# Kernel optimization log

Measured on AMD Instinct MI355X. Metric: run time of the kernel, lower is better.

## Reference

```python
import jax, jax.numpy as jnp
import numpy as np

TAU = 2.0
V_TH = 1.0
V_RESET = 0.0


def setup_inputs() -> dict:
    key = jax.random.key(0)
    k1, k2 = jax.random.split(key)
    T, N, C, H, W = 16, 8, 64, 64, 64
    x_seq = jax.random.normal(k1, (T, N, C, H, W), dtype=jnp.float32)
    conv_weight = jax.random.normal(k2, (C, C, 3, 3), dtype=jnp.float32) * 0.05
    return {"x_seq": x_seq, "conv_weight": conv_weight}


def _conv2d(x, w):
    # x: (B, C, H, W), w: (Cout, Cin, 3, 3), padding=1, no bias
    return jax.lax.conv_general_dilated(
        x, w, window_strides=(1, 1), padding=((1, 1), (1, 1)),
        dimension_numbers=("NCHW", "OIHW", "NCHW"))


def _lif_scan(z_seq):
    # z_seq: (T, N, C, H, W); LIF: decay_input=True, hard reset to V_RESET.
    def step(v, x):
        # charge: v = v + (x - (v - v_reset)) / tau
        v = v + (x - (v - V_RESET)) / TAU
        s = (v >= V_TH).astype(v.dtype)
        # hard reset: v = (1 - s) * v + s * v_reset
        v = (1.0 - s) * v + s * V_RESET
        return v, s

    v0 = jnp.full(z_seq.shape[1:], V_RESET, dtype=z_seq.dtype)
    _, spikes = jax.lax.scan(step, v0, z_seq)
    return spikes


def reference(x_seq, conv_weight):
    T, N = x_seq.shape[:2]
    z = _conv2d(x_seq.reshape(T * N, *x_seq.shape[2:]), conv_weight)
    z = z.reshape(T, N, *z.shape[1:])
    return _lif_scan(z)
```

## Files before the change

kernel.cpp:

```cpp
#include <hip/hip_runtime.h>


namespace {
constexpr int T = 16, N = 8, C = 64, H = 64, W = 64;
constexpr int HW   = H * W;
constexpr int CHW  = C * HW;
constexpr int NCHW = N * CHW;
constexpr int NWT  = C * C * 9;
}

__global__ void wtr_kernel(const float* __restrict__ w, float* __restrict__ wt2) {
    int i = blockIdx.x * 256 + threadIdx.x;
    if (i >= NWT) return;
    int tap  = i % 9;
    int rem  = i / 9;
    int ci   = rem % 64;
    int cout = rem / 64;
    wt2[(tap * 64 + ci) * 64 + cout] = w[i];
}

__global__ __launch_bounds__(256, 6) void conv_kernel(
    const float* __restrict__ x,
    const float* __restrict__ wt2,
    float*       __restrict__ zo)
{
#pragma clang fp contract(off)
    __shared__ float xs[16 * 400];

    const int tid  = threadIdx.x;
    const int wave = __builtin_amdgcn_readfirstlane(tid >> 6);
    const int lane = tid & 63;
    const int px = lane & 7;
    const int py = lane >> 3;
    const int c0 = wave << 4;

    const int bid  = blockIdx.x;
    const int t    = bid >> 9;
    const int r    = bid & 511;
    const int n    = r >> 6;
    const int tile = r & 63;
    const int th0 = (tile >> 3) << 3;
    const int tw0 = (tile & 7) << 3;

    const float* xt = x + (size_t)(t * N + n) * CHW;

#pragma unroll
    for (int it = 0; it < 25; ++it) {
        int j  = tid + it * 256;
        int ci = j / 100;
        int rr = j - ci * 100;
        int dy = rr / 10;
        int dx = rr - dy * 10;
        int hh = th0 - 1 + dy;
        int ww = tw0 - 1 + dx;
        float val = 0.0f;
        if ((unsigned)hh < (unsigned)H && (unsigned)ww < (unsigned)W)
            val = xt[ci * HW + hh * W + ww];
        xs[(ci >> 2) * 400 + rr * 4 + (ci & 3)] = val;
    }
    __syncthreads();

    float acc[16];
#pragma unroll
    for (int i = 0; i < 16; ++i) acc[i] = 0.0f;

    for (int tap = 0; tap < 9; ++tap) {
        const int ky = tap / 3, kx = tap - 3 * ky;
        const int pos = (py + ky) * 10 + (px + kx);
        const float4* xp = (const float4*)xs + pos;
        const float* wtap = wt2 + tap * 4096 + c0;
#pragma unroll 2
        for (int cib = 0; cib < 16; ++cib) {
            const float4 xv = xp[cib * 100];
            const float* wp = wtap + cib * 256;
#pragma unroll
            for (int cc = 0; cc < 16; ++cc)
                acc[cc] = fmaf(wp[cc], xv.x, acc[cc]);
#pragma unroll
            for (int cc = 0; cc < 16; ++cc)
                acc[cc] = fmaf(wp[64 + cc], xv.y, acc[cc]);
#pragma unroll
            for (int cc = 0; cc < 16; ++cc)
                acc[cc] = fmaf(wp[128 + cc], xv.z, acc[cc]);
#pragma unroll
            for (int cc = 0; cc < 16; ++cc)
                acc[cc] = fmaf(wp[192 + cc], xv.w, acc[cc]);
        }
    }

    float* zt = zo + (size_t)(t * N + n) * CHW;
    const int pbase = (th0 + py) * W + (tw0 + px);
#pragma unroll
    for (int cc = 0; cc < 16; ++cc)
        zt[(c0 + cc) * HW + pbase] = acc[cc];
}

__global__ void lif_kernel(float* __restrict__ zo) {
#pragma clang fp contract(off)
    const int gid = blockIdx.x * 256 + threadIdx.x;
    float4 v;
    v.x = 0.0f; v.y = 0.0f; v.z = 0.0f; v.w = 0.0f;
#pragma unroll
    for (int t = 0; t < T; ++t) {
        float4* p = (float4*)(zo + (size_t)t * NCHW) + gid;
        float4 z = *p;
        float4 s;
#define LIF_STEP(comp) { float d = z.comp - v.comp; float hh = d * 0.5f;      \
        v.comp = v.comp + hh;                                                  \
        if (v.comp >= 1.0f) { s.comp = 1.0f; v.comp = 0.0f; }                  \
        else                { s.comp = 0.0f; } }
        LIF_STEP(x) LIF_STEP(y) LIF_STEP(z) LIF_STEP(w)
#undef LIF_STEP
        *p = s;
    }
}

extern "C" void kernel_launch(void* const* d_in, const int* in_sizes, int n_in,
                              void* d_out, int out_size, void* d_ws, size_t ws_size,
                              hipStream_t stream) {
    const float* x = (const float*)d_in[0];
    const float* w = (const float*)d_in[1];
    if (n_in >= 2 && in_sizes[0] < in_sizes[1]) {
        const float* tmp = x; x = w; w = tmp;
    }
    float* out = (float*)d_out;
    float* wt2 = (float*)d_ws;

    wtr_kernel<<<(NWT + 255) / 256, 256, 0, stream>>>(w, wt2);
    conv_kernel<<<T * N * 64, 256, 0, stream>>>(x, wt2, out);
    lif_kernel<<<NCHW / 1024, 256, 0, stream>>>(out);
}
```

Before: 665.1 us.

## Widen conv tile to 8x16 pixels per block and process two float4 per LIF thread

The conv kernel now computes two pixels per thread (8x16 tile per block, half as many blocks), so each weight value loaded is reused across two accumulator sets. This halves weight loads per FMA and reduces halo overhead in shared memory. The cost is higher register pressure (32 accumulators), with launch bounds lowered to 3 blocks per SM. The LIF kernel also gives each thread two float4 streams to raise memory-level parallelism with half the blocks.

```diff
diff --git a/kernel.cpp b/kernel.cpp
--- a/kernel.cpp
+++ b/kernel.cpp
@@ -7,6 +7,7 @@
 constexpr int CHW  = C * HW;
 constexpr int NCHW = N * CHW;
 constexpr int NWT  = C * C * 9;
+constexpr int NPOS = 10 * 18;
 }
 
 __global__ void wtr_kernel(const float* __restrict__ w, float* __restrict__ wt2) {
@@ -19,13 +20,13 @@
     wt2[(tap * 64 + ci) * 64 + cout] = w[i];
 }
 
-__global__ __launch_bounds__(256, 6) void conv_kernel(
+__global__ __launch_bounds__(256, 3) void conv_kernel(
     const float* __restrict__ x,
     const float* __restrict__ wt2,
     float*       __restrict__ zo)
 {
 #pragma clang fp contract(off)
-    __shared__ float xs[16 * 400];
+    __shared__ float xs[16 * NPOS * 4];
 
     const int tid  = threadIdx.x;
     const int wave = __builtin_amdgcn_readfirstlane(tid >> 6);
@@ -35,83 +36,108 @@
     const int c0 = wave << 4;
 
     const int bid  = blockIdx.x;
-    const int t    = bid >> 9;
-    const int r    = bid & 511;
-    const int n    = r >> 6;
-    const int tile = r & 63;
-    const int th0 = (tile >> 3) << 3;
-    const int tw0 = (tile & 7) << 3;
+    const int t    = bid >> 8;
+    const int r    = bid & 255;
+    const int n    = r >> 5;
+    const int tile = r & 31;
+    const int th0 = (tile >> 2) << 3;
+    const int tw0 = (tile & 3) << 4;
 
     const float* xt = x + (size_t)(t * N + n) * CHW;
 
 #pragma unroll
-    for (int it = 0; it < 25; ++it) {
+    for (int it = 0; it < 45; ++it) {
         int j  = tid + it * 256;
-        int ci = j / 100;
-        int rr = j - ci * 100;
-        int dy = rr / 10;
-        int dx = rr - dy * 10;
+        int ci = j / NPOS;
+        int rr = j - ci * NPOS;
+        int dy = rr / 18;
+        int dx = rr - dy * 18;
         int hh = th0 - 1 + dy;
         int ww = tw0 - 1 + dx;
         float val = 0.0f;
         if ((unsigned)hh < (unsigned)H && (unsigned)ww < (unsigned)W)
             val = xt[ci * HW + hh * W + ww];
-        xs[(ci >> 2) * 400 + rr * 4 + (ci & 3)] = val;
+        xs[(ci >> 2) * (NPOS * 4) + rr * 4 + (ci & 3)] = val;
     }
     __syncthreads();
 
-    float acc[16];
+    float acc0[16], acc1[16];
 #pragma unroll
-    for (int i = 0; i < 16; ++i) acc[i] = 0.0f;
+    for (int i = 0; i < 16; ++i) { acc0[i] = 0.0f; acc1[i] = 0.0f; }
 
     for (int tap = 0; tap < 9; ++tap) {
         const int ky = tap / 3, kx = tap - 3 * ky;
-        const int pos = (py + ky) * 10 + (px + kx);
+        const int pos = (py + ky) * 18 + (px + kx);
         const float4* xp = (const float4*)xs + pos;
         const float* wtap = wt2 + tap * 4096 + c0;
 #pragma unroll 2
         for (int cib = 0; cib < 16; ++cib) {
-            const float4 xv = xp[cib * 100];
+            const float4 xv0 = xp[cib * NPOS];
+            const float4 xv1 = xp[cib * NPOS + 8];
             const float* wp = wtap + cib * 256;
 #pragma unroll
-            for (int cc = 0; cc < 16; ++cc)
-                acc[cc] = fmaf(wp[cc], xv.x, acc[cc]);
+            for (int cc = 0; cc < 16; ++cc) {
+                float w0 = wp[cc];
+                acc0[cc] = fmaf(w0, xv0.x, acc0[cc]);
+                acc1[cc] = fmaf(w0, xv1.x, acc1[cc]);
+            }
 #pragma unroll
-            for (int cc = 0; cc < 16; ++cc)
-                acc[cc] = fmaf(wp[64 + cc], xv.y, acc[cc]);
+            for (int cc = 0; cc < 16; ++cc) {
+                float w1 = wp[64 + cc];
+                acc0[cc] = fmaf(w1, xv0.y, acc0[cc]);
+                acc1[cc] = fmaf(w1, xv1.y, acc1[cc]);
+            }
 #pragma unroll
-            for (int cc = 0; cc < 16; ++cc)
-                acc[cc] = fmaf(wp[128 + cc], xv.z, acc[cc]);
+            for (int cc = 0; cc < 16; ++cc) {
+                float w2 = wp[128 + cc];
+                acc0[cc] = fmaf(w2, xv0.z, acc0[cc]);
+                acc1[cc] = fmaf(w2, xv1.z, acc1[cc]);
+            }
 #pragma unroll
-            for (int cc = 0; cc < 16; ++cc)
-                acc[cc] = fmaf(wp[192 + cc], xv.w, acc[cc]);
+            for (int cc = 0; cc < 16; ++cc) {
+                float w3 = wp[192 + cc];
+                acc0[cc] = fmaf(w3, xv0.w, acc0[cc]);
+                acc1[cc] = fmaf(w3, xv1.w, acc1[cc]);
+            }
         }
     }
 
     float* zt = zo + (size_t)(t * N + n) * CHW;
     const int pbase = (th0 + py) * W + (tw0 + px);
 #pragma unroll
-    for (int cc = 0; cc < 16; ++cc)
-        zt[(c0 + cc) * HW + pbase] = acc[cc];
+    for (int cc = 0; cc < 16; ++cc) {
+        zt[(c0 + cc) * HW + pbase]     = acc0[cc];
+        zt[(c0 + cc) * HW + pbase + 8] = acc1[cc];
+    }
 }
 
 __global__ void lif_kernel(float* __restrict__ zo) {
 #pragma clang fp contract(off)
+    constexpr int TOTAL4 = NCHW / 4;
     const int gid = blockIdx.x * 256 + threadIdx.x;
-    float4 v;
-    v.x = 0.0f; v.y = 0.0f; v.z = 0.0f; v.w = 0.0f;
+    const int gid2 = gid + TOTAL4 / 2;
+    float4 va, vb;
+    va.x = va.y = va.z = va.w = 0.0f;
+    vb.x = vb.y = vb.z = vb.w = 0.0f;
 #pragma unroll
     for (int t = 0; t < T; ++t) {
-        float4* p = (float4*)(zo + (size_t)t * NCHW) + gid;
-        float4 z = *p;
-        float4 s;
-#define LIF_STEP(comp) { float d = z.comp - v.comp; float hh = d * 0.5f;      \
-        v.comp = v.comp + hh;                                                  \
+        float4* base = (float4*)(zo + (size_t)t * NCHW);
+        float4* pa = base + gid;
+        float4* pb = base + gid2;
+        float4 za = *pa;
+        float4 zb = *pb;
+        float4 sa, sb;
+#define LIF_STEP(v, z, s, comp) { float d = z.comp - v.comp;                   \
+        float hh = d * 0.5f; v.comp = v.comp + hh;                             \
         if (v.comp >= 1.0f) { s.comp = 1.0f; v.comp = 0.0f; }                  \
         else                { s.comp = 0.0f; } }
-        LIF_STEP(x) LIF_STEP(y) LIF_STEP(z) LIF_STEP(w)
+        LIF_STEP(va, za, sa, x) LIF_STEP(va, za, sa, y)
+        LIF_STEP(va, za, sa, z) LIF_STEP(va, za, sa, w)
+        LIF_STEP(vb, zb, sb, x) LIF_STEP(vb, zb, sb, y)
+        LIF_STEP(vb, zb, sb, z) LIF_STEP(vb, zb, sb, w)
 #undef LIF_STEP
-        *p = s;
+        *pa = sa;
+        *pb = sb;
     }
 }
 
@@ -127,6 +153,6 @@
     float* wt2 = (float*)d_ws;
 
     wtr_kernel<<<(NWT + 255) / 256, 256, 0, stream>>>(w, wt2);
-    conv_kernel<<<T * N * 64, 256, 0, stream>>>(x, wt2, out);
-    lif_kernel<<<NCHW / 1024, 256, 0, stream>>>(out);
+    conv_kernel<<<T * N * 32, 256, 0, stream>>>(x, wt2, out);
+    lif_kernel<<<NCHW / 2048, 256, 0, stream>>>(out);
 }
```

Result: faster. 636.7 us (-4.3%).
